# Kernel optimization log

Measured on AMD Instinct MI355X. Metric: run time of the kernel, lower is better.

The kernel has to match this reference:

```python
import jax, jax.numpy as jnp
import numpy as np
import math

N_HEADS = 4          # h2_dim*n_heads must equal g_dim for the stacked layers
H2_DIM = 32
G_DIM = 128
N_REL = 4
N_LAYERS = 2
PAST_W, FUT_W, PERIODIC = 5, 5, [15]
LN_EPS = 1e-5
BN_EPS = 1e-5


def _build_edges(d):
    ei, et = [], []
    for t in range(d):
        ei.append([t, t]); et.append(0)                      # self-loop
        for off in range(1, PAST_W + 1):
            if t - off >= 0:
                ei.append([t, t - off]); et.append(1)        # past
        for off in range(1, FUT_W + 1):
            if t + off < d:
                ei.append([t, t + off]); et.append(2)        # future
        for off in PERIODIC:
            if t + off < d:
                ei.append([t, t + off]); et.append(3)        # periodic fwd
            if t - off >= 0:
                ei.append([t, t - off]); et.append(3)        # periodic bwd
    return np.array(ei, dtype=np.int64).T, np.array(et, dtype=np.int64)


def setup_inputs() -> dict:
    key = jax.random.key(0)
    b, d, h, w, c = 4, 2048, 8, 8, 192
    ks = jax.random.split(key, 24)
    s = 0.05
    ei, et = _build_edges(d)
    inp = {
        'x': jax.random.normal(ks[0], (b, d, h, w, c), dtype=jnp.float32),
        'edge_index': jnp.asarray(ei),
        'edge_type': jnp.asarray(et),
        'fe_fc_w': jax.random.normal(ks[1], (c, G_DIM), dtype=jnp.float32) * s,
        'fe_fc_b': jnp.zeros((G_DIM,), jnp.float32),
        'fe_ln_g': jnp.ones((G_DIM,), jnp.float32),
        'fe_ln_b': jnp.zeros((G_DIM,), jnp.float32),
        'w_rel': jax.random.normal(ks[2], (N_LAYERS, N_REL, G_DIM, G_DIM), dtype=jnp.float32) * s,
        'w_root': jax.random.normal(ks[3], (N_LAYERS, G_DIM, G_DIM), dtype=jnp.float32) * s,
        'rgcn_b': jnp.zeros((N_LAYERS, G_DIM), jnp.float32),
        'wq': jax.random.normal(ks[4], (N_LAYERS, G_DIM, N_HEADS * H2_DIM), dtype=jnp.float32) * s,
        'bq': jnp.zeros((N_LAYERS, N_HEADS * H2_DIM), jnp.float32),
        'wk': jax.random.normal(ks[5], (N_LAYERS, G_DIM, N_HEADS * H2_DIM), dtype=jnp.float32) * s,
        'bk': jnp.zeros((N_LAYERS, N_HEADS * H2_DIM), jnp.float32),
        'wv': jax.random.normal(ks[6], (N_LAYERS, G_DIM, N_HEADS * H2_DIM), dtype=jnp.float32) * s,
        'bv': jnp.zeros((N_LAYERS, N_HEADS * H2_DIM), jnp.float32),
        'wskip': jax.random.normal(ks[7], (N_LAYERS, G_DIM, N_HEADS * H2_DIM), dtype=jnp.float32) * s,
        'bskip': jnp.zeros((N_LAYERS, N_HEADS * H2_DIM), jnp.float32),
        'bn_g': jnp.ones((N_LAYERS, N_HEADS * H2_DIM), jnp.float32),
        'bn_b': jnp.zeros((N_LAYERS, N_HEADS * H2_DIM), jnp.float32),
    }
    return inp


def _forward(x, edge_index, edge_type, fe_fc_w, fe_fc_b, fe_ln_g, fe_ln_b,
             w_rel, w_root, rgcn_b, wq, bq, wk, bk, wv, bv, wskip, bskip, bn_g, bn_b):
    d = x.shape[1]
    src, dst = edge_index[0], edge_index[1]
    rel_masks = [(edge_type == r).astype(jnp.float32) for r in range(N_REL)]
    inv_sqrt_c = 1.0 / math.sqrt(H2_DIM)

    def graph_fwd(xi):  # xi: [d,h,w,c]
        feat = xi.mean(axis=(1, 2))                         # adaptive avg pool -> [d,c]
        hfe = feat @ fe_fc_w + fe_fc_b                      # [d,g]
        mu = hfe.mean(-1, keepdims=True)
        var = ((hfe - mu) ** 2).mean(-1, keepdims=True)
        nf = (hfe - mu) / jnp.sqrt(var + LN_EPS) * fe_ln_g + fe_ln_b

        for l in range(N_LAYERS):
            # ---- RGCNConv (mean aggregation per relation + root) ----
            out = nf @ w_root[l] + rgcn_b[l]
            for r in range(N_REL):
                m = rel_masks[r]
                xr = nf @ w_rel[l, r]                       # [d,g]
                msg = xr[src] * m[:, None]                  # [E,g]
                s = jax.ops.segment_sum(msg, dst, num_segments=d)
                cnt = jax.ops.segment_sum(m, dst, num_segments=d)
                out = out + s / jnp.maximum(cnt, 1.0)[:, None]
            nf1 = out
            # ---- TransformerConv (per-head edge attention) ----
            q = (nf1 @ wq[l] + bq[l]).reshape(d, N_HEADS, H2_DIM)
            k = (nf1 @ wk[l] + bk[l]).reshape(d, N_HEADS, H2_DIM)
            v = (nf1 @ wv[l] + bv[l]).reshape(d, N_HEADS, H2_DIM)
            logits = (q[dst] * k[src]).sum(-1) * inv_sqrt_c  # [E,H]
            mx = jax.ops.segment_max(logits, dst, num_segments=d)
            a = jnp.exp(logits - mx[dst])
            denom = jax.ops.segment_sum(a, dst, num_segments=d)
            alpha = a / denom[dst]                           # softmax over incoming edges
            agg = jax.ops.segment_sum(alpha[:, :, None] * v[src], dst, num_segments=d)
            out2 = agg.reshape(d, N_HEADS * H2_DIM) + nf1 @ wskip[l] + bskip[l]
            # ---- BatchNorm1d (training-mode batch stats over nodes) ----
            bmu = out2.mean(0)
            bvar = ((out2 - bmu) ** 2).mean(0)
            out2 = (out2 - bmu) / jnp.sqrt(bvar + BN_EPS) * bn_g[l] + bn_b[l]
            nf = jax.nn.leaky_relu(out2, 0.01)
        return nf

    return jax.vmap(graph_fwd)(x)                           # [b,d,g]


def reference(x, edge_index, edge_type, fe_fc_w, fe_fc_b, fe_ln_g, fe_ln_b,
              w_rel, w_root, rgcn_b, wq, bq, wk, bk, wv, bv, wskip, bskip, bn_g, bn_b):
    return _forward(x, edge_index, edge_type, fe_fc_w, fe_fc_b, fe_ln_g, fe_ln_b,
                    w_rel, w_root, rgcn_b, wq, bq, wk, bk, wv, bv, wskip, bskip, bn_g, bn_b)
```

## Files before the change

### kernel.cpp

```cpp
#include <hip/hip_runtime.h>
#include <hip/hip_bf16.h>

#define B_ 4
#define D_ 2048
#define HWS 64
#define C_ 192
#define G_ 128
#define NODES (B_*D_)

typedef short bf8_t  __attribute__((ext_vector_type(8)));
typedef float f32x4_t __attribute__((ext_vector_type(4)));
typedef unsigned short us4_t __attribute__((ext_vector_type(4)));

__device__ inline unsigned short f2bf(float f) {
    unsigned int u = __builtin_bit_cast(unsigned int, f);
    unsigned int r = (u + 0x7fffu + ((u >> 16) & 1u)) >> 16;
    return (unsigned short)r;
}

struct WconvArgs {
    const float* src[16];
    const float* add[16];
};
__global__ __launch_bounds__(256) void wconv_kernel(WconvArgs a, unsigned short* __restrict__ dst)
{
    int m = blockIdx.y;
    int idx = blockIdx.x * 256 + threadIdx.x;
    int n = idx >> 7;
    int k = idx & 127;
    float v = a.src[m][k * G_ + n];
    if (a.add[m]) v += a.add[m][k * G_ + n];
    dst[(size_t)m * 16384 + idx] = f2bf(v);
}

__global__ __launch_bounds__(192) void pool_fc_ln_kernel(
    const float* __restrict__ x, const float* __restrict__ W,
    const float* __restrict__ bias, const float* __restrict__ gam,
    const float* __restrict__ bet, unsigned short* __restrict__ nf)
{
    int u = blockIdx.x;
    int tid = threadIdx.x;
    __shared__ float feat[C_];
    __shared__ float4 red4[4][48];
    __shared__ float red[4];
    __shared__ float stats[2];

    const float4* xb4 = (const float4*)(x + (size_t)u * (HWS * C_));
    int cg = tid % 48;
    int rg = tid / 48;
    float4 a = make_float4(0.f, 0.f, 0.f, 0.f);
    #pragma unroll
    for (int s = 0; s < HWS; s += 4) {
        float4 v = xb4[(size_t)(s + rg) * 48 + cg];
        a.x += v.x; a.y += v.y; a.z += v.z; a.w += v.w;
    }
    red4[rg][cg] = a;
    __syncthreads();
    if (rg == 0) {
        float4 b0 = red4[0][cg], b1 = red4[1][cg], b2 = red4[2][cg], b3 = red4[3][cg];
        feat[cg * 4 + 0] = (b0.x + b1.x + b2.x + b3.x) * (1.0f / HWS);
        feat[cg * 4 + 1] = (b0.y + b1.y + b2.y + b3.y) * (1.0f / HWS);
        feat[cg * 4 + 2] = (b0.z + b1.z + b2.z + b3.z) * (1.0f / HWS);
        feat[cg * 4 + 3] = (b0.w + b1.w + b2.w + b3.w) * (1.0f / HWS);
    }
    __syncthreads();

    float h = 0.f;
    if (tid < G_) {
        h = bias[tid];
        #pragma unroll 4
        for (int c = 0; c < C_; ++c) h += feat[c] * W[c * G_ + tid];
    }
    float s1 = (tid < G_) ? h : 0.f;
    float s2 = (tid < G_) ? h * h : 0.f;
    #pragma unroll
    for (int off = 32; off >= 1; off >>= 1) {
        s1 += __shfl_xor(s1, off, 64);
        s2 += __shfl_xor(s2, off, 64);
    }
    int wid = tid >> 6;
    if ((tid & 63) == 0 && wid < 2) { red[wid] = s1; red[2 + wid] = s2; }
    __syncthreads();
    if (tid == 0) {
        float S = red[0] + red[1];
        float SS = red[2] + red[3];
        float mu = S / G_;
        float var = SS / G_ - mu * mu;
        stats[0] = mu;
        stats[1] = 1.0f / sqrtf(var + 1e-5f);
    }
    __syncthreads();
    if (tid < G_) {
        float v = (h - stats[0]) * stats[1] * gam[tid] + bet[tid];
        nf[(size_t)u * G_ + tid] = f2bf(v);
    }
}

struct GemmMfmaArgs {
    const unsigned short* WT[4];
    const float* bias[4];
    float* Y[4];
};

__global__ __launch_bounds__(256) void gemm_mfma_kernel(
    const unsigned short* __restrict__ A, GemmMfmaArgs args)
{
    int r = blockIdx.y;
    int row0 = blockIdx.x * 64;
    int tid = threadIdx.x;
    __shared__ bf8_t As8[1024];
    char* As = (char*)As8;

    {
        int rowb = tid >> 4;
        int col8 = tid & 15;
        #pragma unroll
        for (int p = 0; p < 4; ++p) {
            int rr = p * 16 + rowb;
            int off = (rr * 256 + col8 * 16) ^ ((rr & 7) << 4);
            *(bf8_t*)(As + off) =
                *(const bf8_t*)(A + (size_t)(row0 + rr) * G_ + col8 * 8);
        }
    }
    __syncthreads();

    int l = tid & 63, wv = tid >> 6;
    int arow = wv * 16 + (l & 15);
    int kgrp = l >> 4;
    bf8_t a[4];
    #pragma unroll
    for (int kc = 0; kc < 4; ++kc) {
        int off = (arow * 256 + kc * 64 + kgrp * 16) ^ ((arow & 7) << 4);
        a[kc] = *(const bf8_t*)(As + off);
    }

    const unsigned short* WTr = args.WT[r];
    f32x4_t acc[8];
    #pragma unroll
    for (int n = 0; n < 8; ++n) acc[n] = (f32x4_t){0.f, 0.f, 0.f, 0.f};

    #pragma unroll
    for (int n = 0; n < 8; ++n) {
        const unsigned short* bp = WTr + (size_t)(n * 16 + (l & 15)) * G_ + kgrp * 8;
        bf8_t b0 = *(const bf8_t*)(bp);
        bf8_t b1 = *(const bf8_t*)(bp + 32);
        bf8_t b2 = *(const bf8_t*)(bp + 64);
        bf8_t b3 = *(const bf8_t*)(bp + 96);
        acc[n] = __builtin_amdgcn_mfma_f32_16x16x32_bf16(a[0], b0, acc[n], 0, 0, 0);
        acc[n] = __builtin_amdgcn_mfma_f32_16x16x32_bf16(a[1], b1, acc[n], 0, 0, 0);
        acc[n] = __builtin_amdgcn_mfma_f32_16x16x32_bf16(a[2], b2, acc[n], 0, 0, 0);
        acc[n] = __builtin_amdgcn_mfma_f32_16x16x32_bf16(a[3], b3, acc[n], 0, 0, 0);
    }

    const float* bias = args.bias[r];
    float* Y = args.Y[r];
    int rbase = row0 + wv * 16 + kgrp * 4;
    #pragma unroll
    for (int n = 0; n < 8; ++n) {
        int col = n * 16 + (l & 15);
        float bb = bias ? bias[col] : 0.f;
        #pragma unroll
        for (int j = 0; j < 4; ++j)
            Y[(size_t)(rbase + j) * G_ + col] = acc[n][j] + bb;
    }
}

__global__ __launch_bounds__(256) void rgcn_stencil_kernel(
    const float* __restrict__ Y, const float* __restrict__ rb,
    unsigned short* __restrict__ out)
{
    int idx = blockIdx.x * 256 + threadIdx.x;
    int g = idx & (G_ - 1);
    int u = idx >> 7;
    int t = u & (D_ - 1);
    const float* Y0 = Y;
    const float* Y1 = Y + (size_t)NODES * G_;
    const float* Y2 = Y1 + (size_t)NODES * G_;
    const float* Y3 = Y2 + (size_t)NODES * G_;

    float acc = Y0[idx] + rb[g];

    float s = 0.f;
    #pragma unroll
    for (int o = 1; o <= 5; ++o) if (t + o < D_) s += Y1[idx + o * G_];
    int c1 = min(5, D_ - 1 - t);
    acc += s / (float)max(c1, 1);

    s = 0.f;
    #pragma unroll
    for (int o = 1; o <= 5; ++o) if (t - o >= 0) s += Y2[idx - o * G_];
    int c2 = min(5, t);
    acc += s / (float)max(c2, 1);

    s = 0.f; int c3 = 0;
    if (t >= 15)     { s += Y3[idx - 15 * G_]; c3++; }
    if (t + 15 < D_) { s += Y3[idx + 15 * G_]; c3++; }
    acc += s / (float)max(c3, 1);

    out[idx] = f2bf(acc);
}

__global__ __launch_bounds__(128) void attn_kernel(
    const float* __restrict__ Q, const float* __restrict__ Kk,
    const float* __restrict__ V, const float* __restrict__ S,
    float* __restrict__ out2)
{
    int u = blockIdx.x;
    int b = u >> 11;
    int t = u & (D_ - 1);
    int j = threadIdx.x;
    const float invs = 0.17677669529663687f;

    int srcs[13];
    srcs[0] = t;
    #pragma unroll
    for (int o = 1; o <= 5; ++o) {
        srcs[o]     = (t + o < D_) ? (t + o) : -1;
        srcs[5 + o] = (t - o >= 0) ? (t - o) : -1;
    }
    srcs[11] = (t >= 15) ? (t - 15) : -1;
    srcs[12] = (t + 15 < D_) ? (t + 15) : -1;

    float q = Q[(size_t)u * G_ + j];
    int base = b << 11;
    float lg[13], vv[13];
    #pragma unroll
    for (int n = 0; n < 13; ++n) {
        int sidx = srcs[n];
        float kk = 0.f, vx = 0.f;
        if (sidx >= 0) {
            size_t off = (size_t)(base + sidx) * G_ + j;
            kk = Kk[off];
            vx = V[off];
        }
        float p = q * kk;
        p += __shfl_xor(p, 16, 32);
        p += __shfl_xor(p, 8, 32);
        p += __shfl_xor(p, 4, 32);
        p += __shfl_xor(p, 2, 32);
        p += __shfl_xor(p, 1, 32);
        lg[n] = (sidx >= 0) ? p * invs : -1e30f;
        vv[n] = vx;
    }
    float m = lg[0];
    #pragma unroll
    for (int n = 1; n < 13; ++n) m = fmaxf(m, lg[n]);
    float den = 0.f, agg = 0.f;
    #pragma unroll
    for (int n = 0; n < 13; ++n) {
        float e = expf(lg[n] - m);
        den += e;
        agg += e * vv[n];
    }
    out2[(size_t)u * G_ + j] = agg / den + S[(size_t)u * G_ + j];
}

__global__ __launch_bounds__(256) void bn_stats_kernel(
    const float* __restrict__ X, float* __restrict__ partials)
{
    int chunk = blockIdx.x;
    int b = blockIdx.y;
    int tid = threadIdx.x;
    const float4* base4 = (const float4*)(X + ((size_t)b * D_ + chunk * 64) * G_);

    float4 s = make_float4(0.f, 0.f, 0.f, 0.f);
    float4 ss = make_float4(0.f, 0.f, 0.f, 0.f);
    #pragma unroll
    for (int p = 0; p < 8; ++p) {
        float4 v = base4[p * 256 + tid];
        s.x += v.x; s.y += v.y; s.z += v.z; s.w += v.w;
        ss.x += v.x * v.x; ss.y += v.y * v.y; ss.z += v.z * v.z; ss.w += v.w * v.w;
    }
    __shared__ float4 rs[8][32], rss[8][32];
    rs[tid >> 5][tid & 31] = s;
    rss[tid >> 5][tid & 31] = ss;
    __syncthreads();
    if (tid < 32) {
        float4 S = make_float4(0.f, 0.f, 0.f, 0.f);
        float4 SS = make_float4(0.f, 0.f, 0.f, 0.f);
        #pragma unroll
        for (int j = 0; j < 8; ++j) {
            float4 a = rs[j][tid], c = rss[j][tid];
            S.x += a.x; S.y += a.y; S.z += a.z; S.w += a.w;
            SS.x += c.x; SS.y += c.y; SS.z += c.z; SS.w += c.w;
        }
        float4* P = (float4*)(partials + ((size_t)b * 32 + chunk) * 256);
        P[tid] = S;
        P[32 + tid] = SS;
    }
}

template <bool BF>
__global__ __launch_bounds__(256) void bn_apply_kernel(
    const float* __restrict__ X, const float* __restrict__ partials,
    const float* __restrict__ gam, const float* __restrict__ bet,
    void* __restrict__ outp)
{
    int chunk = blockIdx.x;
    int b = blockIdx.y;
    int tid = threadIdx.x;
    __shared__ float smu[G_], sinv[G_];
    if (tid < G_) {
        float s = 0.f, ss = 0.f;
        const float* P = partials + (size_t)b * 32 * 256;
        #pragma unroll 4
        for (int k = 0; k < 32; ++k) {
            s += P[k * 256 + tid];
            ss += P[k * 256 + G_ + tid];
        }
        float mu = s / D_;
        float var = ss / D_ - mu * mu;
        smu[tid] = mu;
        sinv[tid] = 1.0f / sqrtf(var + 1e-5f);
    }
    __syncthreads();

    const float4* base4 = (const float4*)(X + ((size_t)b * D_ + chunk * 64) * G_);
    int c4 = (tid & 31) * 4;
    float m0 = smu[c4], m1 = smu[c4 + 1], m2 = smu[c4 + 2], m3 = smu[c4 + 3];
    float i0 = sinv[c4] * gam[c4],     i1 = sinv[c4 + 1] * gam[c4 + 1];
    float i2 = sinv[c4 + 2] * gam[c4 + 2], i3 = sinv[c4 + 3] * gam[c4 + 3];
    float b0 = bet[c4], b1 = bet[c4 + 1], b2 = bet[c4 + 2], b3 = bet[c4 + 3];
    #pragma unroll
    for (int p = 0; p < 8; ++p) {
        float4 v = base4[p * 256 + tid];
        float4 y;
        y.x = (v.x - m0) * i0 + b0;
        y.y = (v.y - m1) * i1 + b1;
        y.z = (v.z - m2) * i2 + b2;
        y.w = (v.w - m3) * i3 + b3;
        y.x = (y.x > 0.f) ? y.x : 0.01f * y.x;
        y.y = (y.y > 0.f) ? y.y : 0.01f * y.y;
        y.z = (y.z > 0.f) ? y.z : 0.01f * y.z;
        y.w = (y.w > 0.f) ? y.w : 0.01f * y.w;
        if constexpr (BF) {
            us4_t o;
            o[0] = f2bf(y.x); o[1] = f2bf(y.y); o[2] = f2bf(y.z); o[3] = f2bf(y.w);
            us4_t* ob = (us4_t*)((unsigned short*)outp + ((size_t)b * D_ + chunk * 64) * G_);
            ob[p * 256 + tid] = o;
        } else {
            float4* ob = (float4*)((float*)outp + ((size_t)b * D_ + chunk * 64) * G_);
            ob[p * 256 + tid] = y;
        }
    }
}

extern "C" void kernel_launch(void* const* d_in, const int* in_sizes, int n_in,
                              void* d_out, int out_size, void* d_ws, size_t ws_size,
                              hipStream_t stream)
{
    (void)in_sizes; (void)n_in; (void)out_size; (void)ws_size;
    const float* x      = (const float*)d_in[0];
    const float* fe_w   = (const float*)d_in[3];
    const float* fe_b   = (const float*)d_in[4];
    const float* ln_g   = (const float*)d_in[5];
    const float* ln_b   = (const float*)d_in[6];
    const float* w_rel  = (const float*)d_in[7];
    const float* w_root = (const float*)d_in[8];
    const float* rgcn_b = (const float*)d_in[9];
    const float* wq  = (const float*)d_in[10];
    const float* bq  = (const float*)d_in[11];
    const float* wk  = (const float*)d_in[12];
    const float* bk  = (const float*)d_in[13];
    const float* wv  = (const float*)d_in[14];
    const float* bv  = (const float*)d_in[15];
    const float* wsk = (const float*)d_in[16];
    const float* bsk = (const float*)d_in[17];
    const float* bn_g = (const float*)d_in[18];
    const float* bn_b = (const float*)d_in[19];

    float* ws   = (float*)d_ws;
    float* Y    = ws;
    float* out2 = Y + (size_t)4 * NODES * G_;
    float* partials = out2 + (size_t)NODES * G_;
    unsigned short* nf_bf = (unsigned short*)(partials + 4 * 32 * 256);
    unsigned short* wbf   = nf_bf + (size_t)NODES * G_;

    WconvArgs wa;
    for (int l = 0; l < 2; ++l) {
        for (int r = 0; r < 4; ++r) {
            wa.src[l * 8 + r] = w_rel + ((size_t)l * 4 + r) * G_ * G_;
            wa.add[l * 8 + r] = (r == 0) ? (w_root + (size_t)l * G_ * G_) : nullptr;
        }
        wa.src[l * 8 + 4] = wq  + (size_t)l * G_ * G_; wa.add[l * 8 + 4] = nullptr;
        wa.src[l * 8 + 5] = wk  + (size_t)l * G_ * G_; wa.add[l * 8 + 5] = nullptr;
        wa.src[l * 8 + 6] = wv  + (size_t)l * G_ * G_; wa.add[l * 8 + 6] = nullptr;
        wa.src[l * 8 + 7] = wsk + (size_t)l * G_ * G_; wa.add[l * 8 + 7] = nullptr;
    }
    wconv_kernel<<<dim3(64, 16), 256, 0, stream>>>(wa, wbf);

    pool_fc_ln_kernel<<<NODES, 192, 0, stream>>>(x, fe_w, fe_b, ln_g, ln_b, nf_bf);

    for (int l = 0; l < 2; ++l) {
        GemmMfmaArgs ga;
        for (int r = 0; r < 4; ++r) {
            ga.WT[r]   = wbf + (size_t)(l * 8 + r) * 16384;
            ga.bias[r] = nullptr;
            ga.Y[r]    = Y + (size_t)r * NODES * G_;
        }
        gemm_mfma_kernel<<<dim3(NODES / 64, 4), 256, 0, stream>>>(nf_bf, ga);

        rgcn_stencil_kernel<<<NODES * G_ / 256, 256, 0, stream>>>(Y, rgcn_b + l * G_, nf_bf);

        GemmMfmaArgs gb;
        gb.WT[0] = wbf + (size_t)(l * 8 + 4) * 16384; gb.bias[0] = bq  + l * G_; gb.Y[0] = Y;
        gb.WT[1] = wbf + (size_t)(l * 8 + 5) * 16384; gb.bias[1] = bk  + l * G_; gb.Y[1] = Y + (size_t)NODES * G_;
        gb.WT[2] = wbf + (size_t)(l * 8 + 6) * 16384; gb.bias[2] = bv  + l * G_; gb.Y[2] = Y + (size_t)2 * NODES * G_;
        gb.WT[3] = wbf + (size_t)(l * 8 + 7) * 16384; gb.bias[3] = bsk + l * G_; gb.Y[3] = Y + (size_t)3 * NODES * G_;
        gemm_mfma_kernel<<<dim3(NODES / 64, 4), 256, 0, stream>>>(nf_bf, gb);

        attn_kernel<<<NODES, 128, 0, stream>>>(
            Y, Y + (size_t)NODES * G_, Y + (size_t)2 * NODES * G_,
            Y + (size_t)3 * NODES * G_, out2);

        bn_stats_kernel<<<dim3(32, 4), 256, 0, stream>>>(out2, partials);
        if (l == 0) {
            bn_apply_kernel<true><<<dim3(32, 4), 256, 0, stream>>>(
                out2, partials, bn_g, bn_b, nf_bf);
        } else {
            bn_apply_kernel<false><<<dim3(32, 4), 256, 0, stream>>>(
                out2, partials, bn_g + G_, bn_b + G_, d_out);
        }
    }
}
```

Before: 254.4 us.

## Fuse RGCN stencil into GEMM and QKV projection with attention and BN stats

Replaces the per-layer pipeline of GEMM, stencil, GEMM, attention and BN-stats kernels with two fused kernels that stage a 32-row tile plus a 15-row halo in shared memory. The first aggregates neighbours before the MFMA GEMM, moving the mean onto the inputs by linearity, so no fp32 Y buffers are written. The second computes Q/K/V/skip projections over the halo, runs the neighbourhood attention from LDS and emits BN partial sums. This removes large fp32 intermediate traffic and several launches, but uses only 256 blocks, so occupancy is lower and the halo K/V are recomputed per block.

```diff
diff --git a/kernel.cpp b/kernel.cpp
--- a/kernel.cpp
+++ b/kernel.cpp
@@ -16,6 +16,10 @@
     unsigned int u = __builtin_bit_cast(unsigned int, f);
     unsigned int r = (u + 0x7fffu + ((u >> 16) & 1u)) >> 16;
     return (unsigned short)r;
+}
+__device__ inline float bf2f(unsigned short h) {
+    unsigned int u = ((unsigned int)h) << 16;
+    return __builtin_bit_cast(float, u);
 }
 
 struct WconvArgs {
@@ -96,197 +100,243 @@
     }
 }
 
-struct GemmMfmaArgs {
-    const unsigned short* WT[4];
-    const float* bias[4];
-    float* Y[4];
-};
-
-__global__ __launch_bounds__(256) void gemm_mfma_kernel(
-    const unsigned short* __restrict__ A, GemmMfmaArgs args)
-{
-    int r = blockIdx.y;
-    int row0 = blockIdx.x * 64;
+__device__ inline void stage_halo(const unsigned short* __restrict__ src,
+                                  int t0, char* raw, int tid)
+{
+    #pragma unroll
+    for (int p = 0; p < 4; ++p) {
+        int task = tid + p * 256;
+        int i = task >> 4, c16 = task & 15;
+        int t = t0 - 15 + i;
+        bf8_t v = {0, 0, 0, 0, 0, 0, 0, 0};
+        if (t >= 0 && t < D_) v = *(const bf8_t*)(src + (size_t)t * G_ + c16 * 8);
+        *(bf8_t*)(raw + ((i * 256 + c16 * 16) ^ ((i & 7) << 4))) = v;
+    }
+}
+
+__global__ __launch_bounds__(256) void rgcn_fused_kernel(
+    const unsigned short* __restrict__ nf,
+    const unsigned short* __restrict__ wt,
+    const float* __restrict__ rb,
+    unsigned short* __restrict__ out)
+{
+    __shared__ char raw[64 * 256];
+    __shared__ char agg[32 * 1024];
+    int blk = blockIdx.x;
+    int b = blk >> 6;
+    int t0 = (blk & 63) * 32;
     int tid = threadIdx.x;
-    __shared__ bf8_t As8[1024];
-    char* As = (char*)As8;
-
-    {
-        int rowb = tid >> 4;
-        int col8 = tid & 15;
-        #pragma unroll
-        for (int p = 0; p < 4; ++p) {
-            int rr = p * 16 + rowb;
-            int off = (rr * 256 + col8 * 16) ^ ((rr & 7) << 4);
-            *(bf8_t*)(As + off) =
-                *(const bf8_t*)(A + (size_t)(row0 + rr) * G_ + col8 * 8);
-        }
+
+    stage_halo(nf + (size_t)b * D_ * G_, t0, raw, tid);
+    __syncthreads();
+
+    #pragma unroll
+    for (int p = 0; p < 8; ++p) {
+        int task = tid + p * 256;
+        int c16 = task & 15, rel = (task >> 4) & 3, row = task >> 6;
+        int t = t0 + row;
+        int ctr = row + 15;
+        float s[8] = {0.f,0.f,0.f,0.f,0.f,0.f,0.f,0.f};
+        float scale = 1.f;
+        if (rel == 0) {
+            bf8_t v = *(const bf8_t*)(raw + ((ctr * 256 + c16 * 16) ^ ((ctr & 7) << 4)));
+            #pragma unroll
+            for (int e = 0; e < 8; ++e) s[e] = bf2f((unsigned short)v[e]);
+        } else if (rel == 1) {
+            #pragma unroll
+            for (int o = 1; o <= 5; ++o) if (t + o < D_) {
+                int i = ctr + o;
+                bf8_t v = *(const bf8_t*)(raw + ((i * 256 + c16 * 16) ^ ((i & 7) << 4)));
+                #pragma unroll
+                for (int e = 0; e < 8; ++e) s[e] += bf2f((unsigned short)v[e]);
+            }
+            scale = 1.f / (float)max(min(5, D_ - 1 - t), 1);
+        } else if (rel == 2) {
+            #pragma unroll
+            for (int o = 1; o <= 5; ++o) if (t - o >= 0) {
+                int i = ctr - o;
+                bf8_t v = *(const bf8_t*)(raw + ((i * 256 + c16 * 16) ^ ((i & 7) << 4)));
+                #pragma unroll
+                for (int e = 0; e < 8; ++e) s[e] += bf2f((unsigned short)v[e]);
+            }
+            scale = 1.f / (float)max(min(5, t), 1);
+        } else {
+            int cnt = 0;
+            if (t >= 15) {
+                int i = row;
+                bf8_t v = *(const bf8_t*)(raw + ((i * 256 + c16 * 16) ^ ((i & 7) << 4)));
+                #pragma unroll
+                for (int e = 0; e < 8; ++e) s[e] += bf2f((unsigned short)v[e]);
+                cnt++;
+            }
+            if (t + 15 < D_) {
+                int i = row + 30;
+                bf8_t v = *(const bf8_t*)(raw + ((i * 256 + c16 * 16) ^ ((i & 7) << 4)));
+                #pragma unroll
+                for (int e = 0; e < 8; ++e) s[e] += bf2f((unsigned short)v[e]);
+                cnt++;
+            }
+            scale = 1.f / (float)max(cnt, 1);
+        }
+        bf8_t o8;
+        #pragma unroll
+        for (int e = 0; e < 8; ++e) o8[e] = (short)f2bf(s[e] * scale);
+        *(bf8_t*)(agg + ((row * 1024 + rel * 256 + c16 * 16) ^ ((row & 7) << 4))) = o8;
     }
     __syncthreads();
 
     int l = tid & 63, wv = tid >> 6;
-    int arow = wv * 16 + (l & 15);
+    int rf = wv & 1, ch2 = wv >> 1;
+    int arow = rf * 16 + (l & 15);
     int kgrp = l >> 4;
-    bf8_t a[4];
-    #pragma unroll
-    for (int kc = 0; kc < 4; ++kc) {
-        int off = (arow * 256 + kc * 64 + kgrp * 16) ^ ((arow & 7) << 4);
-        a[kc] = *(const bf8_t*)(As + off);
-    }
-
-    const unsigned short* WTr = args.WT[r];
-    f32x4_t acc[8];
-    #pragma unroll
-    for (int n = 0; n < 8; ++n) acc[n] = (f32x4_t){0.f, 0.f, 0.f, 0.f};
-
-    #pragma unroll
-    for (int n = 0; n < 8; ++n) {
-        const unsigned short* bp = WTr + (size_t)(n * 16 + (l & 15)) * G_ + kgrp * 8;
-        bf8_t b0 = *(const bf8_t*)(bp);
-        bf8_t b1 = *(const bf8_t*)(bp + 32);
-        bf8_t b2 = *(const bf8_t*)(bp + 64);
-        bf8_t b3 = *(const bf8_t*)(bp + 96);
-        acc[n] = __builtin_amdgcn_mfma_f32_16x16x32_bf16(a[0], b0, acc[n], 0, 0, 0);
-        acc[n] = __builtin_amdgcn_mfma_f32_16x16x32_bf16(a[1], b1, acc[n], 0, 0, 0);
-        acc[n] = __builtin_amdgcn_mfma_f32_16x16x32_bf16(a[2], b2, acc[n], 0, 0, 0);
-        acc[n] = __builtin_amdgcn_mfma_f32_16x16x32_bf16(a[3], b3, acc[n], 0, 0, 0);
-    }
-
-    const float* bias = args.bias[r];
-    float* Y = args.Y[r];
-    int rbase = row0 + wv * 16 + kgrp * 4;
-    #pragma unroll
-    for (int n = 0; n < 8; ++n) {
-        int col = n * 16 + (l & 15);
-        float bb = bias ? bias[col] : 0.f;
+    f32x4_t acc[4];
+    #pragma unroll
+    for (int n = 0; n < 4; ++n) acc[n] = (f32x4_t){0.f, 0.f, 0.f, 0.f};
+
+    for (int ks = 0; ks < 16; ++ks) {
+        int rel = ks >> 2, kk = ks & 3;
+        bf8_t a = *(const bf8_t*)(agg +
+            ((arow * 1024 + rel * 256 + kk * 64 + kgrp * 16) ^ ((arow & 7) << 4)));
+        const unsigned short* wrel = wt + rel * 16384;
+        #pragma unroll
+        for (int n = 0; n < 4; ++n) {
+            int col16 = ch2 * 4 + n;
+            bf8_t bf = *(const bf8_t*)(wrel +
+                (size_t)(col16 * 16 + (l & 15)) * G_ + kk * 32 + kgrp * 8);
+            acc[n] = __builtin_amdgcn_mfma_f32_16x16x32_bf16(a, bf, acc[n], 0, 0, 0);
+        }
+    }
+
+    unsigned short* outb = out + (size_t)b * D_ * G_;
+    int rbase = t0 + rf * 16 + kgrp * 4;
+    #pragma unroll
+    for (int n = 0; n < 4; ++n) {
+        int col = (ch2 * 4 + n) * 16 + (l & 15);
+        float rbv = rb[col];
         #pragma unroll
         for (int j = 0; j < 4; ++j)
-            Y[(size_t)(rbase + j) * G_ + col] = acc[n][j] + bb;
-    }
-}
-
-__global__ __launch_bounds__(256) void rgcn_stencil_kernel(
-    const float* __restrict__ Y, const float* __restrict__ rb,
-    unsigned short* __restrict__ out)
-{
-    int idx = blockIdx.x * 256 + threadIdx.x;
-    int g = idx & (G_ - 1);
-    int u = idx >> 7;
-    int t = u & (D_ - 1);
-    const float* Y0 = Y;
-    const float* Y1 = Y + (size_t)NODES * G_;
-    const float* Y2 = Y1 + (size_t)NODES * G_;
-    const float* Y3 = Y2 + (size_t)NODES * G_;
-
-    float acc = Y0[idx] + rb[g];
-
-    float s = 0.f;
-    #pragma unroll
-    for (int o = 1; o <= 5; ++o) if (t + o < D_) s += Y1[idx + o * G_];
-    int c1 = min(5, D_ - 1 - t);
-    acc += s / (float)max(c1, 1);
-
-    s = 0.f;
-    #pragma unroll
-    for (int o = 1; o <= 5; ++o) if (t - o >= 0) s += Y2[idx - o * G_];
-    int c2 = min(5, t);
-    acc += s / (float)max(c2, 1);
-
-    s = 0.f; int c3 = 0;
-    if (t >= 15)     { s += Y3[idx - 15 * G_]; c3++; }
-    if (t + 15 < D_) { s += Y3[idx + 15 * G_]; c3++; }
-    acc += s / (float)max(c3, 1);
-
-    out[idx] = f2bf(acc);
-}
-
-__global__ __launch_bounds__(128) void attn_kernel(
-    const float* __restrict__ Q, const float* __restrict__ Kk,
-    const float* __restrict__ V, const float* __restrict__ S,
-    float* __restrict__ out2)
-{
-    int u = blockIdx.x;
-    int b = u >> 11;
-    int t = u & (D_ - 1);
-    int j = threadIdx.x;
+            outb[(size_t)(rbase + j) * G_ + col] = f2bf(acc[n][j] + rbv);
+    }
+}
+
+__global__ __launch_bounds__(256) void qkvs_attn_kernel(
+    const unsigned short* __restrict__ nf1,
+    const unsigned short* __restrict__ wt,
+    const float* __restrict__ bq, const float* __restrict__ bk,
+    const float* __restrict__ bv, const float* __restrict__ bsk,
+    float* __restrict__ out2, float* __restrict__ partials)
+{
+    __shared__ char raw[64 * 256];
+    __shared__ unsigned short kls[64 * 128];
+    __shared__ unsigned short vls[64 * 128];
+    __shared__ unsigned short qls[32 * 128];
+    __shared__ float sls[32 * 128];
+    int blk = blockIdx.x, tid = threadIdx.x;
+    int b = blk >> 6, t0 = (blk & 63) * 32;
+
+    stage_halo(nf1 + (size_t)b * D_ * G_, t0, raw, tid);
+    __syncthreads();
+
+    int l = tid & 63, wvid = tid >> 6, kgrp = l >> 4;
+    #pragma unroll
+    for (int i = 0; i < 3; ++i) {
+        int job = wvid + i * 4;
+        int m, frag;
+        if (job < 4)       { m = 1; frag = job; }
+        else if (job < 8)  { m = 2; frag = job - 4; }
+        else if (job < 10) { m = 0; frag = job - 8; }
+        else               { m = 3; frag = job - 10; }
+        int rawrow = ((m == 1) | (m == 2)) ? (frag * 16 + (l & 15))
+                                           : (15 + frag * 16 + (l & 15));
+        const unsigned short* wm = wt + (size_t)m * 16384;
+        const float* bias = (m == 0) ? bq : (m == 1) ? bk : (m == 2) ? bv : bsk;
+
+        bf8_t a[4];
+        #pragma unroll
+        for (int kc = 0; kc < 4; ++kc)
+            a[kc] = *(const bf8_t*)(raw +
+                ((rawrow * 256 + kc * 64 + kgrp * 16) ^ ((rawrow & 7) << 4)));
+        f32x4_t acc[8];
+        #pragma unroll
+        for (int n = 0; n < 8; ++n) acc[n] = (f32x4_t){0.f, 0.f, 0.f, 0.f};
+        #pragma unroll
+        for (int kc = 0; kc < 4; ++kc) {
+            #pragma unroll
+            for (int n = 0; n < 8; ++n) {
+                bf8_t bf = *(const bf8_t*)(wm +
+                    (size_t)(n * 16 + (l & 15)) * G_ + kc * 32 + kgrp * 8);
+                acc[n] = __builtin_amdgcn_mfma_f32_16x16x32_bf16(a[kc], bf, acc[n], 0, 0, 0);
+            }
+        }
+        int r0 = frag * 16 + kgrp * 4;
+        #pragma unroll
+        for (int n = 0; n < 8; ++n) {
+            int col = n * 16 + (l & 15);
+            float bb = bias[col];
+            #pragma unroll
+            for (int j = 0; j < 4; ++j) {
+                float v = acc[n][j] + bb;
+                int rr = r0 + j;
+                if (m == 1)      kls[rr * 128 + col] = f2bf(v);
+                else if (m == 2) vls[rr * 128 + col] = f2bf(v);
+                else if (m == 0) qls[rr * 128 + col] = f2bf(v);
+                else             sls[rr * 128 + col] = v;
+            }
+        }
+    }
+    __syncthreads();
+
+    int j = tid & 127, half = tid >> 7;
     const float invs = 0.17677669529663687f;
-
-    int srcs[13];
-    srcs[0] = t;
-    #pragma unroll
-    for (int o = 1; o <= 5; ++o) {
-        srcs[o]     = (t + o < D_) ? (t + o) : -1;
-        srcs[5 + o] = (t - o >= 0) ? (t - o) : -1;
-    }
-    srcs[11] = (t >= 15) ? (t - 15) : -1;
-    srcs[12] = (t + 15 < D_) ? (t + 15) : -1;
-
-    float q = Q[(size_t)u * G_ + j];
-    int base = b << 11;
-    float lg[13], vv[13];
-    #pragma unroll
-    for (int n = 0; n < 13; ++n) {
-        int sidx = srcs[n];
-        float kk = 0.f, vx = 0.f;
-        if (sidx >= 0) {
-            size_t off = (size_t)(base + sidx) * G_ + j;
-            kk = Kk[off];
-            vx = V[off];
-        }
-        float p = q * kk;
-        p += __shfl_xor(p, 16, 32);
-        p += __shfl_xor(p, 8, 32);
-        p += __shfl_xor(p, 4, 32);
-        p += __shfl_xor(p, 2, 32);
-        p += __shfl_xor(p, 1, 32);
-        lg[n] = (sidx >= 0) ? p * invs : -1e30f;
-        vv[n] = vx;
-    }
-    float m = lg[0];
-    #pragma unroll
-    for (int n = 1; n < 13; ++n) m = fmaxf(m, lg[n]);
-    float den = 0.f, agg = 0.f;
-    #pragma unroll
-    for (int n = 0; n < 13; ++n) {
-        float e = expf(lg[n] - m);
-        den += e;
-        agg += e * vv[n];
-    }
-    out2[(size_t)u * G_ + j] = agg / den + S[(size_t)u * G_ + j];
-}
-
-__global__ __launch_bounds__(256) void bn_stats_kernel(
-    const float* __restrict__ X, float* __restrict__ partials)
-{
-    int chunk = blockIdx.x;
-    int b = blockIdx.y;
-    int tid = threadIdx.x;
-    const float4* base4 = (const float4*)(X + ((size_t)b * D_ + chunk * 64) * G_);
-
-    float4 s = make_float4(0.f, 0.f, 0.f, 0.f);
-    float4 ss = make_float4(0.f, 0.f, 0.f, 0.f);
-    #pragma unroll
-    for (int p = 0; p < 8; ++p) {
-        float4 v = base4[p * 256 + tid];
-        s.x += v.x; s.y += v.y; s.z += v.z; s.w += v.w;
-        ss.x += v.x * v.x; ss.y += v.y * v.y; ss.z += v.z * v.z; ss.w += v.w * v.w;
-    }
-    __shared__ float4 rs[8][32], rss[8][32];
-    rs[tid >> 5][tid & 31] = s;
-    rss[tid >> 5][tid & 31] = ss;
-    __syncthreads();
-    if (tid < 32) {
-        float4 S = make_float4(0.f, 0.f, 0.f, 0.f);
-        float4 SS = make_float4(0.f, 0.f, 0.f, 0.f);
-        #pragma unroll
-        for (int j = 0; j < 8; ++j) {
-            float4 a = rs[j][tid], c = rss[j][tid];
-            S.x += a.x; S.y += a.y; S.z += a.z; S.w += a.w;
-            SS.x += c.x; SS.y += c.y; SS.z += c.z; SS.w += c.w;
-        }
-        float4* P = (float4*)(partials + ((size_t)b * 32 + chunk) * 256);
-        P[tid] = S;
-        P[32 + tid] = SS;
+    float ps = 0.f, pss = 0.f;
+    float* o2b = out2 + (size_t)b * D_ * G_;
+    const int offs[13] = {0, 1, 2, 3, 4, 5, -1, -2, -3, -4, -5, -15, 15};
+    for (int it = 0; it < 16; ++it) {
+        int tl = it * 2 + half;
+        int t = t0 + tl;
+        float q = bf2f(qls[tl * 128 + j]);
+        float lg[13], vv[13];
+        #pragma unroll
+        for (int n = 0; n < 13; ++n) {
+            int ts = t + offs[n];
+            bool ok = (ts >= 0) && (ts < D_);
+            int ki = tl + 15 + offs[n];
+            float kk = ok ? bf2f(kls[ki * 128 + j]) : 0.f;
+            vv[n] = ok ? bf2f(vls[ki * 128 + j]) : 0.f;
+            float p = q * kk;
+            p += __shfl_xor(p, 16, 32);
+            p += __shfl_xor(p, 8, 32);
+            p += __shfl_xor(p, 4, 32);
+            p += __shfl_xor(p, 2, 32);
+            p += __shfl_xor(p, 1, 32);
+            lg[n] = ok ? p * invs : -1e30f;
+        }
+        float m = lg[0];
+        #pragma unroll
+        for (int n = 1; n < 13; ++n) m = fmaxf(m, lg[n]);
+        float den = 0.f, aggv = 0.f;
+        #pragma unroll
+        for (int n = 0; n < 13; ++n) {
+            float e = expf(lg[n] - m);
+            den += e;
+            aggv += e * vv[n];
+        }
+        float o = aggv / den + sls[tl * 128 + j];
+        o2b[(size_t)t * G_ + j] = o;
+        ps += o; pss += o * o;
+    }
+
+    __syncthreads();
+    float* red = (float*)raw;
+    red[half * 128 + j] = ps;
+    red[256 + half * 128 + j] = pss;
+    __syncthreads();
+    if (tid < 128) {
+        float s = red[j] + red[128 + j];
+        float ss = red[256 + j] + red[384 + j];
+        float* P = partials + ((size_t)b * 64 + (blk & 63)) * 256;
+        P[j] = s;
+        P[128 + j] = ss;
     }
 }
 
@@ -302,9 +352,9 @@
     __shared__ float smu[G_], sinv[G_];
     if (tid < G_) {
         float s = 0.f, ss = 0.f;
-        const float* P = partials + (size_t)b * 32 * 256;
+        const float* P = partials + (size_t)b * 64 * 256;
         #pragma unroll 4
-        for (int k = 0; k < 32; ++k) {
+        for (int k = 0; k < 64; ++k) {
             s += P[k * 256 + tid];
             ss += P[k * 256 + G_ + tid];
         }
@@ -370,11 +420,11 @@
     const float* bn_b = (const float*)d_in[19];
 
     float* ws   = (float*)d_ws;
-    float* Y    = ws;
-    float* out2 = Y + (size_t)4 * NODES * G_;
+    float* out2 = ws;
     float* partials = out2 + (size_t)NODES * G_;
-    unsigned short* nf_bf = (unsigned short*)(partials + 4 * 32 * 256);
-    unsigned short* wbf   = nf_bf + (size_t)NODES * G_;
+    unsigned short* nf_bf  = (unsigned short*)(partials + 4 * 64 * 256);
+    unsigned short* nf1_bf = nf_bf + (size_t)NODES * G_;
+    unsigned short* wbf    = nf1_bf + (size_t)NODES * G_;
 
     WconvArgs wa;
     for (int l = 0; l < 2; ++l) {
@@ -392,28 +442,14 @@
     pool_fc_ln_kernel<<<NODES, 192, 0, stream>>>(x, fe_w, fe_b, ln_g, ln_b, nf_bf);
 
     for (int l = 0; l < 2; ++l) {
-        GemmMfmaArgs ga;
-        for (int r = 0; r < 4; ++r) {
-            ga.WT[r]   = wbf + (size_t)(l * 8 + r) * 16384;
-            ga.bias[r] = nullptr;
-            ga.Y[r]    = Y + (size_t)r * NODES * G_;
-        }
-        gemm_mfma_kernel<<<dim3(NODES / 64, 4), 256, 0, stream>>>(nf_bf, ga);
-
-        rgcn_stencil_kernel<<<NODES * G_ / 256, 256, 0, stream>>>(Y, rgcn_b + l * G_, nf_bf);
-
-        GemmMfmaArgs gb;
-        gb.WT[0] = wbf + (size_t)(l * 8 + 4) * 16384; gb.bias[0] = bq  + l * G_; gb.Y[0] = Y;
-        gb.WT[1] = wbf + (size_t)(l * 8 + 5) * 16384; gb.bias[1] = bk  + l * G_; gb.Y[1] = Y + (size_t)NODES * G_;
-        gb.WT[2] = wbf + (size_t)(l * 8 + 6) * 16384; gb.bias[2] = bv  + l * G_; gb.Y[2] = Y + (size_t)2 * NODES * G_;
-        gb.WT[3] = wbf + (size_t)(l * 8 + 7) * 16384; gb.bias[3] = bsk + l * G_; gb.Y[3] = Y + (size_t)3 * NODES * G_;
-        gemm_mfma_kernel<<<dim3(NODES / 64, 4), 256, 0, stream>>>(nf_bf, gb);
-
-        attn_kernel<<<NODES, 128, 0, stream>>>(
-            Y, Y + (size_t)NODES * G_, Y + (size_t)2 * NODES * G_,
-            Y + (size_t)3 * NODES * G_, out2);
-
-        bn_stats_kernel<<<dim3(32, 4), 256, 0, stream>>>(out2, partials);
+        rgcn_fused_kernel<<<256, 256, 0, stream>>>(
+            nf_bf, wbf + (size_t)l * 8 * 16384, rgcn_b + l * G_, nf1_bf);
+
+        qkvs_attn_kernel<<<256, 256, 0, stream>>>(
+            nf1_bf, wbf + (size_t)(l * 8 + 4) * 16384,
+            bq + l * G_, bk + l * G_, bv + l * G_, bsk + l * G_,
+            out2, partials);
+
         if (l == 0) {
             bn_apply_kernel<true><<<dim3(32, 4), 256, 0, stream>>>(
                 out2, partials, bn_g, bn_b, nf_bf);
```

Result: slower. 310.2 us (+22.0%).
